# Optimization experiments

Hardware: AMD Instinct MI355X
Metric: run time of the kernel (lower is better)

The kernel has to match this reference:

```python
import jax, jax.numpy as jnp
import numpy as np

B, R, L, F, H = 65536, 12, 16, 8, 64  # batch, rss_dim, n_leds, led_feat_dim, head_dim

def setup_inputs() -> dict:
    key = jax.random.key(0)
    ks = jax.random.split(key, 20)
    p = lambda k, shp, s=0.1: (jax.random.normal(k, shp, dtype=jnp.float32) * s)
    return {
        "rss_t": jax.random.uniform(ks[0], (B, R, 1), dtype=jnp.float32),
        "led_features": jax.random.normal(ks[1], (B, L, F), dtype=jnp.float32),
        "led_positions": jax.random.normal(ks[2], (B, L, 3), dtype=jnp.float32),
        "prev_pos": jax.random.normal(ks[3], (B, 3), dtype=jnp.float32),
        "freq_mask": jax.random.randint(ks[4], (R, L), 0, 2).astype(jnp.int32),
        # intensity_gate: Linear(1,16) -> ReLU -> Linear(16,1) -> Sigmoid
        "gw1": p(ks[5], (1, 16)), "gb1": p(ks[6], (16,)),
        "gw2": p(ks[7], (16, 1)), "gb2": p(ks[8], (1,)),
        # query_proj: Linear(1,32) -> ReLU -> Linear(32,64)
        "qw1": p(ks[9], (1, 32)), "qb1": p(ks[10], (32,)),
        "qw2": p(ks[11], (32, H)), "qb2": p(ks[12], (H,)),
        # key_proj: Linear(F+3,32) -> ReLU -> Linear(32,64)
        "kw1": p(ks[13], (F + 3, 32)), "kb1": p(ks[14], (32,)),
        "kw2": p(ks[15], (32, H)), "kb2": p(ks[16], (H,)),
        "sigma": jnp.float32(0.5),
    }

def reference(rss_t, led_features, led_positions, prev_pos, freq_mask,
              gw1, gb1, gw2, gb2, qw1, qb1, qw2, qb2, kw1, kb1, kw2, kb2, sigma):
    # intensity gate with hard threshold
    gate = jax.nn.sigmoid(jax.nn.relu(rss_t @ gw1 + gb1) @ gw2 + gb2)  # [B,R,1]
    iw = (rss_t > 0.5).astype(rss_t.dtype) * gate                      # [B,R,1]
    # query / key projections
    Q = jax.nn.relu((rss_t * iw) @ qw1 + qb1) @ qw2 + qb2              # [B,R,H]
    led_input = jnp.concatenate([led_features, led_positions], axis=-1)  # [B,L,F+3]
    K = jax.nn.relu(led_input @ kw1 + kb1) @ kw2 + kb2                 # [B,L,H]
    scores = jnp.einsum("brh,blh->brl", Q, K)                          # [B,R,L]
    # distance bias
    dist_sq = jnp.sum((prev_pos[:, None, :] - led_positions) ** 2, axis=-1)  # [B,L]
    scores = scores - dist_sq[:, None, :] / (2.0 * sigma ** 2)
    # mask + softmax
    neg = jnp.finfo(scores.dtype).min
    scores = jnp.where(freq_mask[None, :, :] == 0, neg, scores)
    attn = jax.nn.softmax(scores, axis=-1)                             # [B,R,L]
    return attn, iw.squeeze(-1)
```

## Files before the change

### kernel.cpp

```cpp
#include <hip/hip_runtime.h>

#define B_TOT 65536
#define R 12
#define L 16
#define NB 16
#define NEG_MIN -3.402823466e38f

#define WS_V   0
#define WS_C   32
#define WS_PM  40
#define WS_BP  64
#define WS_TAB 96
#define TROW   72
#define WS_WF  2472

#define WROWS (4 * 16 * 24 + 8)

typedef __attribute__((ext_vector_type(8))) short short8;
typedef __attribute__((ext_vector_type(4))) float f32x4;

static __device__ __forceinline__ short f2bf(float f) {
    uint32_t u = __float_as_uint(f);
    uint32_t r = u + 0x7FFFu + ((u >> 16) & 1u);
    return (short)(r >> 16);
}

static __device__ __forceinline__ unsigned cvt_pk_bf16(float a, float b) {
    unsigned d;
    asm("v_cvt_pk_bf16_f32 %0, %1, %2" : "=v"(d) : "v"(a), "v"(b));
    return d;
}

__global__ __launch_bounds__(256) void nfh_pre(
    const float* __restrict__ qw1, const float* __restrict__ qb1,
    const float* __restrict__ qw2, const float* __restrict__ qb2,
    const float* __restrict__ kw2, const float* __restrict__ kb2,
    const float* __restrict__ kw1, const float* __restrict__ kb1,
    const int*   __restrict__ fmask,
    float* __restrict__ ws)
{
    __shared__ float sM[1024];
    __shared__ float su[32];
    __shared__ float sw1[32], sb1[32], sbp[32], sbq[32];
    const int t = threadIdx.x;

    if (t < 32) { sw1[t] = qw1[t]; sb1[t] = qb1[t]; }
    for (int e = t; e < 1024; e += 256) {
        const int i = e >> 5, j = e & 31;
        float acc = 0.f;
        for (int h = 0; h < 64; ++h) acc = fmaf(qw2[i * 64 + h], kw2[j * 64 + h], acc);
        sM[e] = acc;
    }
    if (t < 32) {
        float au = 0.f, av = 0.f;
        for (int h = 0; h < 64; ++h) {
            au = fmaf(qw2[t * 64 + h], kb2[h], au);
            av = fmaf(kw2[t * 64 + h], qb2[h], av);
        }
        su[t] = au;
        ws[WS_V + t] = av;
        const float w = qw1[t];
        sbp[t] = (w != 0.f) ? (-qb1[t] / w) : 3.0e30f;
    }
    if (t == 64) {
        float acc = 0.f;
        for (int h = 0; h < 64; ++h) acc = fmaf(qb2[h], kb2[h], acc);
        ws[WS_C] = acc;
    }
    if (t < 12) {
        int pm = 0;
        for (int l = 0; l < 16; ++l) if (fmask[t * 16 + l] != 0) pm |= (1 << l);
        ((int*)ws)[WS_PM + t] = pm;
    }
    __syncthreads();
    if (t < 32) {
        const float key = sbp[t];
        int rank = 0;
        #pragma unroll
        for (int i = 0; i < 32; ++i) {
            const float vi = sbp[i];
            rank += (vi < key || (vi == key && i < t)) ? 1 : 0;
        }
        sbq[rank] = key;
    }
    __syncthreads();
    if (t < 32) ws[WS_BP + t] = sbq[t];

    for (int task = t; task < 33 * 32 + 33; task += 256) {
        const int m = (task < 33 * 32) ? (task >> 5) : (task - 33 * 32);
        const float xi = (m == 0) ? sbq[0] - 1.f
                       : ((m == 32) ? sbq[31] + 1.f
                                    : sbq[m - 1] + 0.5f * (sbq[m] - sbq[m - 1]));
        if (task < 33 * 32) {
            const int j = task & 31;
            float A = 0.f, Bv = 0.f;
            for (int i = 0; i < 32; ++i) {
                if (fmaf(sw1[i], xi, sb1[i]) > 0.f) {
                    A  = fmaf(sw1[i], sM[i * 32 + j], A);
                    Bv = fmaf(sb1[i], sM[i * 32 + j], Bv);
                }
            }
            ws[WS_TAB + m * TROW + j] = A;
            ws[WS_TAB + m * TROW + 36 + j] = Bv;
        } else {
            float Au = 0.f, Bu = 0.f;
            for (int i = 0; i < 32; ++i) {
                if (fmaf(sw1[i], xi, sb1[i]) > 0.f) {
                    Au = fmaf(sw1[i], su[i], Au);
                    Bu = fmaf(sb1[i], su[i], Bu);
                }
            }
            ws[WS_TAB + m * TROW + 32] = Au;
            ws[WS_TAB + m * TROW + 36 + 32] = Bu;
        }
    }

    {
        const int fr = t >> 6;
        const int li = t & 63;
        const int jl = li & 15, kb = li >> 4;
        const int T = fr & 1, term = fr >> 1;
        const int q = ((jl >> 2) << 3) + (T << 2) + (jl & 3);
        short* wsp = (short*)(ws + WS_WF);
        #pragma unroll
        for (int e = 0; e < 8; ++e) {
            const int k = kb * 8 + e;
            float w = 0.f;
            if (term == 0) {
                if (k < 11)       w = kw1[k * 32 + q];
                else if (k == 11) w = kb1[q];
            } else {
                if (k < 11)       { const float a = kw1[k * 32 + q];
                                    w = a - __uint_as_float(((uint32_t)(uint16_t)f2bf(a)) << 16); }
                else if (k == 11) { const float b = kb1[q];
                                    w = b - __uint_as_float(((uint32_t)(uint16_t)f2bf(b)) << 16); }
                else if (k < 23)  w = kw1[(k - 12) * 32 + q];
            }
            wsp[(fr * 64 + li) * 8 + e] = f2bf(w);
        }
    }
}

__global__ __launch_bounds__(256, 8) void nfh_main(
    const float* __restrict__ rss,
    const float* __restrict__ feat,
    const float* __restrict__ pos,
    const float* __restrict__ prev,
    const float* __restrict__ gw1, const float* __restrict__ gb1,
    const float* __restrict__ gw2, const float* __restrict__ gb2,
    const float* __restrict__ sigma_p,
    const float* __restrict__ ws,
    float* __restrict__ out)
{
    __shared__ short s_in[4 * WROWS];

    const int t = threadIdx.x;
    const int lane = t & 63;
    const int wv = t >> 6;
    const int lg = lane >> 4;
    const int b0 = blockIdx.x * NB;
    const float sigma = sigma_p[0];
    const float inv2s2 = 1.f / (2.f * sigma * sigma);

    const short* wsp = (const short*)(ws + WS_WF);
    const short8 wf0 = *(const short8*)(wsp + (0 * 64 + lane) * 8);
    const short8 wf1 = *(const short8*)(wsp + (1 * 64 + lane) * 8);
    const short8 wf2 = *(const short8*)(wsp + (2 * 64 + lane) * 8);
    const short8 wf3 = *(const short8*)(wsp + (3 * 64 + lane) * 8);
    const f32x4 v0 = *(const f32x4*)(ws + WS_V + lg * 8);
    const f32x4 v1 = *(const f32x4*)(ws + WS_V + lg * 8 + 4);
    const float cconst = ws[WS_C];

    if (lane < 8) s_in[wv * WROWS + 4 * 16 * 24 + lane] = 0;

    float my_dq;
    {
        const int bb1 = t >> 4, l1 = t & 15;
        const int b = b0 + bb1;
        float in[12];
        const float4* f4 = (const float4*)(feat + ((size_t)b * (L * 8) + l1 * 8));
        const float4 fa = f4[0], fb = f4[1];
        in[0] = fa.x; in[1] = fa.y; in[2] = fa.z; in[3] = fa.w;
        in[4] = fb.x; in[5] = fb.y; in[6] = fb.z; in[7] = fb.w;
        const float* pp = pos + ((size_t)b * (L * 3) + l1 * 3);
        in[8] = pp[0]; in[9] = pp[1]; in[10] = pp[2];
        in[11] = 1.0f;

        float dsq = 0.f;
        #pragma unroll
        for (int m = 0; m < 3; ++m) {
            const float d = prev[b * 3 + m] - in[8 + m];
            dsq = fmaf(d, d, dsq);
        }
        my_dq = cconst - dsq * inv2s2;

        unsigned hp[6], lp[6];
        #pragma unroll
        for (int p = 0; p < 6; ++p) {
            const float a = in[2 * p], c = in[2 * p + 1];
            const unsigned h = cvt_pk_bf16(a, c);
            hp[p] = h;
            const float h0 = __uint_as_float(h << 16);
            const float h1 = __uint_as_float(h & 0xFFFF0000u);
            lp[p] = cvt_pk_bf16(a - h0, c - h1);
        }

        uint4* rowp = (uint4*)&s_in[wv * WROWS + ((bb1 & 3) * 16 + l1) * 24];
        rowp[0] = make_uint4(hp[0], hp[1], hp[2], hp[3]);
        rowp[1] = make_uint4(hp[4], hp[5], lp[0], lp[1]);
        rowp[2] = make_uint4(lp[2], lp[3], lp[4], lp[5]);
    }

    float my_xq = 0.f;
    {
        const int bb2 = t >> 4;
        const int r2 = t & 15;
        if (r2 < R) {
            const int b = b0 + bb2;
            const float x = rss[(size_t)b * R + r2];
            float z = gb2[0];
            #pragma unroll
            for (int i = 0; i < 16; ++i) {
                const float h = fmaxf(fmaf(x, gw1[i], gb1[i]), 0.f);
                z = fmaf(h, gw2[i], z);
            }
            const float gate = 1.f / (1.f + __expf(-z));
            const float iw = (x > 0.5f) ? gate : 0.f;
            out[(size_t)B_TOT * R * L + (size_t)b * R + r2] = iw;
            my_xq = x * iw;
        }
    }
    int my_k = 0;
    #pragma unroll
    for (int m = 0; m < 32; ++m) my_k += (my_xq > ws[WS_BP + m]) ? 1 : 0;
    const float* myrow = ws + WS_TAB + my_k * TROW;
    const float my_tc = fmaf(my_xq, myrow[32], myrow[68]);

    asm volatile("s_waitcnt lgkmcnt(0)" ::: "memory");

    {
        const int r = lane & 15;
        const int pm = (r < R) ? ((const int*)ws)[WS_PM + r] : 0;
        const int j0 = lg * 8;

        #pragma unroll 1
        for (int i = 0; i < 4; ++i) {
            const int bb = wv * 4 + i;
            const int src = i * 16 + r;
            const float xq_s = __shfl(my_xq, src);
            const int   k_s  = __shfl(my_k,  src);
            const float tc_s = __shfl(my_tc, src);
            const float dq_s = __shfl(my_dq, src);

            const short8 i1 = *(const short8*)(&s_in[wv * WROWS + (i * 16 + r) * 24] + j0);

            f32x4 d0 = {0.f, 0.f, 0.f, 0.f};
            f32x4 d1 = {0.f, 0.f, 0.f, 0.f};
            d0 = __builtin_amdgcn_mfma_f32_16x16x32_bf16(wf0, i1, d0, 0, 0, 0);
            d0 = __builtin_amdgcn_mfma_f32_16x16x32_bf16(wf2, i1, d0, 0, 0, 0);
            d1 = __builtin_amdgcn_mfma_f32_16x16x32_bf16(wf1, i1, d1, 0, 0, 0);
            d1 = __builtin_amdgcn_mfma_f32_16x16x32_bf16(wf3, i1, d1, 0, 0, 0);

            float vbp = 0.f;
            #pragma unroll
            for (int j = 0; j < 4; ++j) {
                d0[j] = fmaxf(d0[j], 0.f);
                vbp = fmaf(v0[j], d0[j], vbp);
            }
            #pragma unroll
            for (int j = 0; j < 4; ++j) {
                d1[j] = fmaxf(d1[j], 0.f);
                vbp = fmaf(v1[j], d1[j], vbp);
            }
            vbp += __shfl_xor(vbp, 16);
            vbp += __shfl_xor(vbp, 32);
            const float vbl = vbp + dq_s;

            uint4 afp;
            afp.x = cvt_pk_bf16(d0[0], d0[1]);
            afp.y = cvt_pk_bf16(d0[2], d0[3]);
            afp.z = cvt_pk_bf16(d1[0], d1[1]);
            afp.w = cvt_pk_bf16(d1[2], d1[3]);
            const short8 af = *(const short8*)&afp;

            const float* rowt = ws + WS_TAB + k_s * TROW;
            const float4 a0 = *(const float4*)(rowt + j0);
            const float4 a1 = *(const float4*)(rowt + j0 + 4);
            const float4 c0 = *(const float4*)(rowt + 36 + j0);
            const float4 c1 = *(const float4*)(rowt + 36 + j0 + 4);
            uint4 bfp;
            bfp.x = cvt_pk_bf16(fmaf(xq_s, a0.x, c0.x), fmaf(xq_s, a0.y, c0.y));
            bfp.y = cvt_pk_bf16(fmaf(xq_s, a0.z, c0.z), fmaf(xq_s, a0.w, c0.w));
            bfp.z = cvt_pk_bf16(fmaf(xq_s, a1.x, c1.x), fmaf(xq_s, a1.y, c1.y));
            bfp.w = cvt_pk_bf16(fmaf(xq_s, a1.z, c1.z), fmaf(xq_s, a1.w, c1.w));
            const short8 bf = *(const short8*)&bfp;

            f32x4 acc = {0.f, 0.f, 0.f, 0.f};
            acc = __builtin_amdgcn_mfma_f32_16x16x32_bf16(af, bf, acc, 0, 0, 0);

            float sc[4];
            #pragma unroll
            for (int j = 0; j < 4; ++j) {
                const float vbj = __shfl(vbl, lg * 4 + j);
                sc[j] = acc[j] + tc_s + vbj;
                if (!((pm >> (lg * 4 + j)) & 1)) sc[j] = NEG_MIN;
            }
            float mx = fmaxf(fmaxf(sc[0], sc[1]), fmaxf(sc[2], sc[3]));
            mx = fmaxf(mx, __shfl_xor(mx, 16));
            mx = fmaxf(mx, __shfl_xor(mx, 32));
            float sum = 0.f;
            #pragma unroll
            for (int j = 0; j < 4; ++j) { sc[j] = __expf(sc[j] - mx); sum += sc[j]; }
            sum += __shfl_xor(sum, 16);
            sum += __shfl_xor(sum, 32);
            const float inv = 1.f / sum;

            if (r < R) {
                float4* op = (float4*)(out + ((size_t)(b0 + bb) * R + r) * L + lg * 4);
                *op = make_float4(sc[0] * inv, sc[1] * inv, sc[2] * inv, sc[3] * inv);
            }
        }
    }
}

extern "C" void kernel_launch(void* const* d_in, const int* in_sizes, int n_in,
                              void* d_out, int out_size, void* d_ws, size_t ws_size,
                              hipStream_t stream) {
    const float* rss   = (const float*)d_in[0];
    const float* feat  = (const float*)d_in[1];
    const float* pos   = (const float*)d_in[2];
    const float* prev  = (const float*)d_in[3];
    const int*   fmask = (const int*)d_in[4];
    const float* gw1   = (const float*)d_in[5];
    const float* gb1   = (const float*)d_in[6];
    const float* gw2   = (const float*)d_in[7];
    const float* gb2   = (const float*)d_in[8];
    const float* qw1   = (const float*)d_in[9];
    const float* qb1   = (const float*)d_in[10];
    const float* qw2   = (const float*)d_in[11];
    const float* qb2   = (const float*)d_in[12];
    const float* kw1   = (const float*)d_in[13];
    const float* kb1   = (const float*)d_in[14];
    const float* kw2   = (const float*)d_in[15];
    const float* kb2   = (const float*)d_in[16];
    const float* sigma = (const float*)d_in[17];
    float* out = (float*)d_out;
    float* ws  = (float*)d_ws;

    nfh_pre<<<1, 256, 0, stream>>>(qw1, qb1, qw2, qb2, kw2, kb2, kw1, kb1, fmask, ws);
    nfh_main<<<B_TOT / NB, 256, 0, stream>>>(
        rss, feat, pos, prev,
        gw1, gb1, gw2, gb2,
        sigma, ws, out);
}
```

Measured before the change: 166.1 us.

## Process eight batch rows per wave with all global loads hoisted upfront

```diff
diff --git a/kernel.cpp b/kernel.cpp
--- a/kernel.cpp
+++ b/kernel.cpp
@@ -3,7 +3,7 @@
 #define B_TOT 65536
 #define R 12
 #define L 16
-#define NB 16
+#define NB 32
 #define NEG_MIN -3.402823466e38f
 
 #define WS_V   0
@@ -14,7 +14,7 @@
 #define TROW   72
 #define WS_WF  2472
 
-#define WROWS (4 * 16 * 24 + 8)
+#define WROWS (8 * 16 * 24 + 8)
 
 typedef __attribute__((ext_vector_type(8))) short short8;
 typedef __attribute__((ext_vector_type(4))) float f32x4;
@@ -141,7 +141,7 @@
     }
 }
 
-__global__ __launch_bounds__(256, 8) void nfh_main(
+__global__ __launch_bounds__(256) void nfh_main(
     const float* __restrict__ rss,
     const float* __restrict__ feat,
     const float* __restrict__ pos,
@@ -159,6 +159,7 @@
     const int wv = t >> 6;
     const int lg = lane >> 4;
     const int b0 = blockIdx.x * NB;
+    const int bw = b0 + wv * 8;
     const float sigma = sigma_p[0];
     const float inv2s2 = 1.f / (2.f * sigma * sigma);
 
@@ -171,28 +172,39 @@
     const f32x4 v1 = *(const f32x4*)(ws + WS_V + lg * 8 + 4);
     const float cconst = ws[WS_C];
 
-    if (lane < 8) s_in[wv * WROWS + 4 * 16 * 24 + lane] = 0;
-
-    float my_dq;
+    if (lane < 8) s_in[wv * WROWS + 8 * 16 * 24 + lane] = 0;
+
+    const int l1 = lane & 15;
+    const int bl = lane >> 4;
+    const int b_p0 = bw + bl, b_p1 = bw + 4 + bl;
+
+    const float4* f40 = (const float4*)(feat + ((size_t)b_p0 * (L * 8) + l1 * 8));
+    const float4* f41 = (const float4*)(feat + ((size_t)b_p1 * (L * 8) + l1 * 8));
+    const float4 fa0 = f40[0], fb0 = f40[1];
+    const float4 fa1 = f41[0], fb1 = f41[1];
+    const float* pp0 = pos + ((size_t)b_p0 * (L * 3) + l1 * 3);
+    const float* pp1 = pos + ((size_t)b_p1 * (L * 3) + l1 * 3);
+    const float px0 = pp0[0], py0 = pp0[1], pz0 = pp0[2];
+    const float px1 = pp1[0], py1 = pp1[1], pz1 = pp1[2];
+    const float qx0 = prev[b_p0 * 3], qy0 = prev[b_p0 * 3 + 1], qz0 = prev[b_p0 * 3 + 2];
+    const float qx1 = prev[b_p1 * 3], qy1 = prev[b_p1 * 3 + 1], qz1 = prev[b_p1 * 3 + 2];
+    float x0 = 0.f, x1 = 0.f;
+    if (l1 < R) {
+        x0 = rss[(size_t)b_p0 * R + l1];
+        x1 = rss[(size_t)b_p1 * R + l1];
+    }
+
+    float my_dq0, my_dq1;
     {
-        const int bb1 = t >> 4, l1 = t & 15;
-        const int b = b0 + bb1;
         float in[12];
-        const float4* f4 = (const float4*)(feat + ((size_t)b * (L * 8) + l1 * 8));
-        const float4 fa = f4[0], fb = f4[1];
-        in[0] = fa.x; in[1] = fa.y; in[2] = fa.z; in[3] = fa.w;
-        in[4] = fb.x; in[5] = fb.y; in[6] = fb.z; in[7] = fb.w;
-        const float* pp = pos + ((size_t)b * (L * 3) + l1 * 3);
-        in[8] = pp[0]; in[9] = pp[1]; in[10] = pp[2];
-        in[11] = 1.0f;
-
+        in[0] = fa0.x; in[1] = fa0.y; in[2] = fa0.z; in[3] = fa0.w;
+        in[4] = fb0.x; in[5] = fb0.y; in[6] = fb0.z; in[7] = fb0.w;
+        in[8] = px0; in[9] = py0; in[10] = pz0; in[11] = 1.0f;
         float dsq = 0.f;
-        #pragma unroll
-        for (int m = 0; m < 3; ++m) {
-            const float d = prev[b * 3 + m] - in[8 + m];
-            dsq = fmaf(d, d, dsq);
-        }
-        my_dq = cconst - dsq * inv2s2;
+        dsq = fmaf(qx0 - px0, qx0 - px0, dsq);
+        dsq = fmaf(qy0 - py0, qy0 - py0, dsq);
+        dsq = fmaf(qz0 - pz0, qz0 - pz0, dsq);
+        my_dq0 = cconst - dsq * inv2s2;
 
         unsigned hp[6], lp[6];
         #pragma unroll
@@ -204,37 +216,67 @@
             const float h1 = __uint_as_float(h & 0xFFFF0000u);
             lp[p] = cvt_pk_bf16(a - h0, c - h1);
         }
-
-        uint4* rowp = (uint4*)&s_in[wv * WROWS + ((bb1 & 3) * 16 + l1) * 24];
+        uint4* rowp = (uint4*)&s_in[wv * WROWS + (bl * 16 + l1) * 24];
         rowp[0] = make_uint4(hp[0], hp[1], hp[2], hp[3]);
         rowp[1] = make_uint4(hp[4], hp[5], lp[0], lp[1]);
         rowp[2] = make_uint4(lp[2], lp[3], lp[4], lp[5]);
     }
-
-    float my_xq = 0.f;
     {
-        const int bb2 = t >> 4;
-        const int r2 = t & 15;
-        if (r2 < R) {
-            const int b = b0 + bb2;
-            const float x = rss[(size_t)b * R + r2];
-            float z = gb2[0];
-            #pragma unroll
-            for (int i = 0; i < 16; ++i) {
-                const float h = fmaxf(fmaf(x, gw1[i], gb1[i]), 0.f);
-                z = fmaf(h, gw2[i], z);
-            }
-            const float gate = 1.f / (1.f + __expf(-z));
-            const float iw = (x > 0.5f) ? gate : 0.f;
-            out[(size_t)B_TOT * R * L + (size_t)b * R + r2] = iw;
-            my_xq = x * iw;
-        }
-    }
-    int my_k = 0;
+        float in[12];
+        in[0] = fa1.x; in[1] = fa1.y; in[2] = fa1.z; in[3] = fa1.w;
+        in[4] = fb1.x; in[5] = fb1.y; in[6] = fb1.z; in[7] = fb1.w;
+        in[8] = px1; in[9] = py1; in[10] = pz1; in[11] = 1.0f;
+        float dsq = 0.f;
+        dsq = fmaf(qx1 - px1, qx1 - px1, dsq);
+        dsq = fmaf(qy1 - py1, qy1 - py1, dsq);
+        dsq = fmaf(qz1 - pz1, qz1 - pz1, dsq);
+        my_dq1 = cconst - dsq * inv2s2;
+
+        unsigned hp[6], lp[6];
+        #pragma unroll
+        for (int p = 0; p < 6; ++p) {
+            const float a = in[2 * p], c = in[2 * p + 1];
+            const unsigned h = cvt_pk_bf16(a, c);
+            hp[p] = h;
+            const float h0 = __uint_as_float(h << 16);
+            const float h1 = __uint_as_float(h & 0xFFFF0000u);
+            lp[p] = cvt_pk_bf16(a - h0, c - h1);
+        }
+        uint4* rowp = (uint4*)&s_in[wv * WROWS + ((bl + 4) * 16 + l1) * 24];
+        rowp[0] = make_uint4(hp[0], hp[1], hp[2], hp[3]);
+        rowp[1] = make_uint4(hp[4], hp[5], lp[0], lp[1]);
+        rowp[2] = make_uint4(lp[2], lp[3], lp[4], lp[5]);
+    }
+
+    float my_xq0 = 0.f, my_xq1 = 0.f;
+    if (l1 < R) {
+        float z0 = gb2[0], z1 = gb2[0];
+        #pragma unroll
+        for (int i = 0; i < 16; ++i) {
+            const float w1 = gw1[i], bb1_ = gb1[i], w2 = gw2[i];
+            z0 = fmaf(fmaxf(fmaf(x0, w1, bb1_), 0.f), w2, z0);
+            z1 = fmaf(fmaxf(fmaf(x1, w1, bb1_), 0.f), w2, z1);
+        }
+        const float g0 = 1.f / (1.f + __expf(-z0));
+        const float g1 = 1.f / (1.f + __expf(-z1));
+        const float iw0 = (x0 > 0.5f) ? g0 : 0.f;
+        const float iw1 = (x1 > 0.5f) ? g1 : 0.f;
+        out[(size_t)B_TOT * R * L + (size_t)b_p0 * R + l1] = iw0;
+        out[(size_t)B_TOT * R * L + (size_t)b_p1 * R + l1] = iw1;
+        my_xq0 = x0 * iw0;
+        my_xq1 = x1 * iw1;
+    }
+    int my_k0 = 0, my_k1 = 0;
     #pragma unroll
-    for (int m = 0; m < 32; ++m) my_k += (my_xq > ws[WS_BP + m]) ? 1 : 0;
-    const float* myrow = ws + WS_TAB + my_k * TROW;
-    const float my_tc = fmaf(my_xq, myrow[32], myrow[68]);
+    for (int m = 0; m < 32; ++m) {
+        const float bp = ws[WS_BP + m];
+        my_k0 += (my_xq0 > bp) ? 1 : 0;
+        my_k1 += (my_xq1 > bp) ? 1 : 0;
+    }
+    const float* myrow0 = ws + WS_TAB + my_k0 * TROW;
+    const float* myrow1 = ws + WS_TAB + my_k1 * TROW;
+    const float my_tc0 = fmaf(my_xq0, myrow0[32], myrow0[68]);
+    const float my_tc1 = fmaf(my_xq1, myrow1[32], myrow1[68]);
 
     asm volatile("s_waitcnt lgkmcnt(0)" ::: "memory");
 
@@ -243,14 +285,14 @@
         const int pm = (r < R) ? ((const int*)ws)[WS_PM + r] : 0;
         const int j0 = lg * 8;
 
-        #pragma unroll 1
-        for (int i = 0; i < 4; ++i) {
-            const int bb = wv * 4 + i;
-            const int src = i * 16 + r;
-            const float xq_s = __shfl(my_xq, src);
-            const int   k_s  = __shfl(my_k,  src);
-            const float tc_s = __shfl(my_tc, src);
-            const float dq_s = __shfl(my_dq, src);
+        #pragma unroll 2
+        for (int i = 0; i < 8; ++i) {
+            const int src = ((i & 3) << 4) | r;
+            const bool hi = (i >= 4);
+            const float xq_s = __shfl(hi ? my_xq1 : my_xq0, src);
+            const int   k_s  = __shfl(hi ? my_k1  : my_k0,  src);
+            const float tc_s = __shfl(hi ? my_tc1 : my_tc0, src);
+            const float dq_s = __shfl(hi ? my_dq1 : my_dq0, src);
 
             const short8 i1 = *(const short8*)(&s_in[wv * WROWS + (i * 16 + r) * 24] + j0);
 
@@ -316,7 +358,7 @@
             const float inv = 1.f / sum;
 
             if (r < R) {
-                float4* op = (float4*)(out + ((size_t)(b0 + bb) * R + r) * L + lg * 4);
+                float4* op = (float4*)(out + ((size_t)(bw + i) * R + r) * L + lg * 4);
                 *op = make_float4(sc[0] * inv, sc[1] * inv, sc[2] * inv, sc[3] * inv);
             }
         }
```

After: 164.8 us. About the same (-0.8%).
